# Performance work log

Measured on AMD Instinct MI355X. Metric: run time of the kernel, lower is better.

Reference implementation:

```python
import jax, jax.numpy as jnp
import numpy as np

B, S, DIM = 1, 2048, 4096
N_HEADS, N_KV_HEADS = 32, 8
HEAD_DIM = DIM // N_HEADS            # 128
N_REP = N_HEADS // N_KV_HEADS        # 4
Q_SIZE = N_HEADS * HEAD_DIM          # 4096
KV_SIZE = N_KV_HEADS * HEAD_DIM      # 1024


def setup_inputs() -> dict:
    key = jax.random.key(0)
    ks = jax.random.split(key, 5)
    x = jax.random.normal(ks[0], (B, S, DIM), dtype=jnp.float32)
    # RoPE tables: freqs_cis[s, j] = exp(i * s * theta_j), theta_j = 10000^(-2j/head_dim)
    theta = 10000.0 ** (-jnp.arange(0, HEAD_DIM, 2, dtype=jnp.float32) / HEAD_DIM)
    ang = jnp.arange(S, dtype=jnp.float32)[:, None] * theta[None, :]  # [S, HEAD_DIM//2]
    freqs_cos = jnp.cos(ang)
    freqs_sin = jnp.sin(ang)
    # causal additive mask [1,1,S,S]
    causal = jnp.tril(jnp.ones((S, S), dtype=bool))
    mask = jnp.where(causal, 0.0, -1e9).astype(jnp.float32)[None, None]
    wqkv = jax.random.normal(ks[1], (Q_SIZE + 2 * KV_SIZE, DIM), dtype=jnp.float32) * (DIM ** -0.5)
    wo = jax.random.normal(ks[2], (DIM, Q_SIZE), dtype=jnp.float32) * (Q_SIZE ** -0.5)
    return {"x": x, "freqs_cos": freqs_cos, "freqs_sin": freqs_sin, "mask": mask,
            "wqkv": wqkv, "wo": wo}


def _apply_rope(t, cos, sin):
    # t: [B, S, H, D]; cos/sin: [S, D//2]  (complex multiply on (even, odd) pairs)
    b, s, h, d = t.shape
    tp = t.reshape(b, s, h, d // 2, 2)
    t0, t1 = tp[..., 0], tp[..., 1]
    c = cos[None, :, None, :]
    sn = sin[None, :, None, :]
    out = jnp.stack([t0 * c - t1 * sn, t0 * sn + t1 * c], axis=-1)
    return out.reshape(b, s, h, d)


def reference(x, freqs_cos, freqs_sin, mask, wqkv, wo):
    bsz, seqlen, _ = x.shape
    qkv = jnp.einsum('bsd,od->bso', x, wqkv)  # fused QKV projection
    xq = qkv[..., :Q_SIZE].reshape(bsz, seqlen, N_HEADS, HEAD_DIM)
    xk = qkv[..., Q_SIZE:Q_SIZE + KV_SIZE].reshape(bsz, seqlen, N_KV_HEADS, HEAD_DIM)
    xv = qkv[..., Q_SIZE + KV_SIZE:].reshape(bsz, seqlen, N_KV_HEADS, HEAD_DIM)
    # rotary embedding on q, k
    xq = _apply_rope(xq, freqs_cos, freqs_sin)
    xk = _apply_rope(xk, freqs_cos, freqs_sin)
    # cache insertion (prefill: cache == current k/v), layout [B, KVH, S, D]
    cache_k = jnp.swapaxes(xk, 1, 2)
    cache_v = jnp.swapaxes(xv, 1, 2)
    # GQA repeat_kv -> [B, H, S, D]
    keys = jnp.repeat(cache_k, N_REP, axis=1)
    values = jnp.repeat(cache_v, N_REP, axis=1)
    # scores: einsum 'ijkl,ikml->ikjm' with xq [b,s,h,d], keys [b,h,t,d] -> [b,h,s,t]
    scores = jnp.einsum('bshd,bhtd->bhst', xq, keys) / jnp.sqrt(jnp.float32(HEAD_DIM))
    scores = scores + mask
    scores = jax.nn.softmax(scores.astype(jnp.float32), axis=-1).astype(xq.dtype)
    out = jnp.einsum('bhst,bhtd->bhsd', scores, values)  # [B, H, S, D]
    out = jnp.swapaxes(out, 1, 2).reshape(bsz, seqlen, Q_SIZE)
    return jnp.einsum('bso,do->bsd', out, wo)
```

## Files before the change

### kernel.cpp

```cpp
#include <hip/hip_runtime.h>
#include <hip/hip_bf16.h>
#include <cstdint>
#include <cstddef>


typedef __attribute__((ext_vector_type(4)))  float    f32x4;
typedef __attribute__((ext_vector_type(16))) float    f32x16;
typedef __attribute__((ext_vector_type(8)))  __bf16   bf16x8;
typedef __attribute__((ext_vector_type(4)))  __bf16   bf16x4;
typedef __attribute__((ext_vector_type(2)))  __bf16   bf16x2;
typedef __attribute__((ext_vector_type(4)))  uint32_t u32x4;

typedef const __attribute__((address_space(1))) void* gaddr_t;
typedef __attribute__((address_space(3))) void*       laddr_t;

#define S_LEN   2048
#define DIM_    4096
#define NHEADS  32
#define NKV     8
#define HD      128
#define QKV_LD  6144
#define KOFF    4096
#define VOFF    5120

#define EXP2F(x) __builtin_amdgcn_exp2f(x)

__global__ void cvt_f32_bf16(const float* __restrict__ in, __bf16* __restrict__ out, int n4) {
  int idx = blockIdx.x * blockDim.x + threadIdx.x;
  int stride = gridDim.x * blockDim.x;
  for (int i = idx; i < n4; i += stride) {
    float4 v = reinterpret_cast<const float4*>(in)[i];
    bf16x4 o;
    o[0] = (__bf16)v.x; o[1] = (__bf16)v.y; o[2] = (__bf16)v.z; o[3] = (__bf16)v.w;
    reinterpret_cast<bf16x4*>(out)[i] = o;
  }
}

__global__ void rope_kernel(__bf16* __restrict__ qkv, const float* __restrict__ fc,
                            const float* __restrict__ fs) {
  int tid = blockIdx.x * 256 + threadIdx.x;
  int i = tid & 63;
  int t = tid >> 6;
  int h = t % 40;
  int s = t / 40;
  int col = (h < NHEADS) ? (h * HD + 2 * i) : (KOFF + (h - NHEADS) * HD + 2 * i);
  size_t off = (size_t)s * QKV_LD + col;
  float c = fc[s * 64 + i], sn = fs[s * 64 + i];
  bf16x2 v = *reinterpret_cast<bf16x2*>(&qkv[off]);
  float t0 = (float)v[0], t1 = (float)v[1];
  bf16x2 o;
  o[0] = (__bf16)(t0 * c - t1 * sn);
  o[1] = (__bf16)(t0 * sn + t1 * c);
  *reinterpret_cast<bf16x2*>(&qkv[off]) = o;
}

__device__ __forceinline__ void stage64x(const __bf16* __restrict__ P, int ld, int row0,
                                         int kt, char* dst, int tid) {
#pragma unroll
  for (int j = 0; j < 2; ++j) {
    int c = j * 256 + tid;
    int r = c >> 3, g = c & 7;
    const __bf16* src = P + (size_t)(row0 + r) * ld + kt * 64 + ((g ^ (r & 7)) * 8);
    __builtin_amdgcn_global_load_lds((gaddr_t)src,
        (laddr_t)(dst + j * 4096 + (tid & ~63) * 16), 16, 0, 0);
  }
}

template <int KH, bool VM>
__device__ __forceinline__ void phase32(const __bf16* __restrict__ Ab,
                                        const __bf16* __restrict__ Bb,
                                        f32x16 (&acc)[2][2],
                                        int wm, int wn, int l31, int hi, int tid,
                                        const __bf16* __restrict__ SP, int sld,
                                        int srow0, char* sdst, int kt, bool st) {
  bf16x8 af[2][2], bfr[2][2];
#pragma unroll
  for (int mi = 0; mi < 2; ++mi) {
    int R = wm * 64 + mi * 32 + l31;
#pragma unroll
    for (int k2 = 0; k2 < 2; ++k2)
      af[mi][k2] = *reinterpret_cast<const bf16x8*>(
          (const char*)Ab + R * 128 + (((KH * 4 + k2 * 2 + hi) ^ (R & 7)) * 16));
  }
#pragma unroll
  for (int ni = 0; ni < 2; ++ni) {
    int R = wn * 64 + ni * 32 + l31;
#pragma unroll
    for (int k2 = 0; k2 < 2; ++k2)
      bfr[ni][k2] = *reinterpret_cast<const bf16x8*>(
          (const char*)Bb + R * 128 + (((KH * 4 + k2 * 2 + hi) ^ (R & 7)) * 16));
  }
  if (st) {
    stage64x(SP, sld, srow0, kt, sdst, tid);
    stage64x(SP, sld, srow0 + 64, kt, sdst + 8192, tid);
  }
  __builtin_amdgcn_s_barrier();
  asm volatile("s_waitcnt lgkmcnt(0)" ::: "memory");
  __builtin_amdgcn_sched_barrier(0);
  __builtin_amdgcn_s_setprio(1);
#pragma unroll
  for (int k2 = 0; k2 < 2; ++k2)
#pragma unroll
    for (int mi = 0; mi < 2; ++mi)
#pragma unroll
      for (int ni = 0; ni < 2; ++ni)
        acc[mi][ni] = __builtin_amdgcn_mfma_f32_32x32x16_bf16(af[mi][k2], bfr[ni][k2],
                                                              acc[mi][ni], 0, 0, 0);
  __builtin_amdgcn_s_setprio(0);
  if (VM) asm volatile("s_waitcnt vmcnt(0)" ::: "memory");
  __builtin_amdgcn_s_barrier();
}

template <int MB, int NPX, typename OutT>
__global__ __launch_bounds__(256, 2) void gemm32(const __bf16* __restrict__ A,
                                                 const __bf16* __restrict__ B,
                                                 OutT* __restrict__ C, int K,
                                                 int lda, int ldb, int ldc) {
  __shared__ __align__(16) __bf16 As[2][128 * 64];
  __shared__ __align__(16) __bf16 Bs[2][128 * 64];
  const int tid = threadIdx.x;
  const int lane = tid & 63, l31 = lane & 31, hi = lane >> 5, w = tid >> 6;
  const int wm = w >> 1, wn = w & 1;
  const int bid = blockIdx.x, xcd = bid & 7, lid = bid >> 3;
  const int m0 = (lid % MB) * 128;
  const int n0 = (xcd * NPX + lid / MB) * 128;

  f32x16 acc[2][2] = {};

  stage64x(A, lda, m0, 0, (char*)As[0], tid);
  stage64x(A, lda, m0 + 64, 0, (char*)As[0] + 8192, tid);
  stage64x(B, ldb, n0, 0, (char*)Bs[0], tid);
  stage64x(B, ldb, n0 + 64, 0, (char*)Bs[0] + 8192, tid);
  asm volatile("s_waitcnt vmcnt(0)" ::: "memory");
  __builtin_amdgcn_s_barrier();

  const int ntiles = K >> 6;
  for (int t = 0; t < ntiles; ++t) {
    const int cur = t & 1;
    const __bf16* Ab = As[cur];
    const __bf16* Bb = Bs[cur];
    char* dA = (char*)As[1 - cur];
    char* dB = (char*)Bs[1 - cur];
    const bool st = (t + 1 < ntiles);
    phase32<0, false>(Ab, Bb, acc, wm, wn, l31, hi, tid, A, lda, m0, dA, t + 1, st);
    phase32<1, true >(Ab, Bb, acc, wm, wn, l31, hi, tid, B, ldb, n0, dB, t + 1, st);
  }

#pragma unroll
  for (int mi = 0; mi < 2; ++mi)
#pragma unroll
    for (int ni = 0; ni < 2; ++ni)
#pragma unroll
      for (int e = 0; e < 16; ++e) {
        int row = m0 + wm * 64 + mi * 32 + (e & 3) + 8 * (e >> 2) + 4 * hi;
        int col = n0 + wn * 64 + ni * 32 + l31;
        C[(size_t)row * ldc + col] = (OutT)acc[mi][ni][e];
      }
}

__device__ inline uint32_t pack2(float a, float b) {
  bf16x2 t; t[0] = (__bf16)a; t[1] = (__bf16)b;
  return __builtin_bit_cast(uint32_t, t);
}

__global__ __launch_bounds__(256, 2) void attn_kernel(const __bf16* __restrict__ qkv,
                                                      __bf16* __restrict__ out) {
  __shared__ __align__(16) __bf16 Ks[2][64 * 128];
  __shared__ __align__(16) __bf16 Vt[2][128][72];
  const int tid = threadIdx.x;
  const int lane = tid & 63, l31 = lane & 31, hi = lane >> 5, wq = tid >> 6;
  const int head = blockIdx.x & 31;
  const int g = blockIdx.x >> 5;
  const int qt = (g < 8) ? (15 - g) : (g - 8);
  const int q0 = qt * 128;
  const int nt = 2 * qt + 2;
  const int kvh = head >> 2;
  const float sc2 = 0.08838834764831845f * 1.44269504089f;
  const int qr = q0 + wq * 32 + l31;

  bf16x8 vr[2][2];

  auto stage_k = [&](int tt, int buf) {
#pragma unroll
    for (int i = 0; i < 4; ++i) {
      int c = i * 256 + tid;
      int r = c >> 4, gg = c & 15;
      const __bf16* gk = qkv + (size_t)(tt * 64 + r) * QKV_LD + KOFF + kvh * HD + ((gg ^ (r & 7)) * 8);
      __builtin_amdgcn_global_load_lds((gaddr_t)gk,
          (laddr_t)((char*)Ks[buf] + (tid & ~63) * 16 + i * 4096), 16, 0, 0);
    }
  };
  auto load_v = [&](int tt) {
#pragma unroll
    for (int i = 0; i < 2; ++i) {
      int task = i * 256 + tid;
      int p = task >> 4, cg = task & 15;
      const __bf16* vp = qkv + (size_t)(tt * 64 + 2 * p) * QKV_LD + VOFF + kvh * HD + cg * 8;
      vr[i][0] = *reinterpret_cast<const bf16x8*>(vp);
      vr[i][1] = *reinterpret_cast<const bf16x8*>(vp + QKV_LD);
    }
  };
  auto write_v = [&](int buf) {
#pragma unroll
    for (int i = 0; i < 2; ++i) {
      int task = i * 256 + tid;
      int p = task >> 4, cg = task & 15;
#pragma unroll
      for (int e0 = 0; e0 < 8; ++e0) {
        int e = e0 ^ (lane & 7);
        bf16x2 pkv; pkv[0] = vr[i][0][e]; pkv[1] = vr[i][1][e];
        *reinterpret_cast<bf16x2*>(&Vt[buf][cg * 8 + e][2 * p]) = pkv;
      }
    }
  };

  bf16x8 qf[8];
  {
    const __bf16* qp = qkv + (size_t)qr * QKV_LD + head * HD + hi * 8;
#pragma unroll
    for (int ks = 0; ks < 8; ++ks) qf[ks] = *reinterpret_cast<const bf16x8*>(qp + ks * 16);
  }
  f32x16 o[4] = {};
  float m_run = -3e38f, l_run = 0.f;

  stage_k(0, 0); load_v(0); write_v(0);

  for (int t = 0; t < nt; ++t) {
    const int cur = t & 1;
    __syncthreads();
    if (t + 1 < nt) { stage_k(t + 1, 1 - cur); load_v(t + 1); }

    f32x16 st[2];
#pragma unroll
    for (int sub = 0; sub < 2; ++sub) {
      f32x16 acc = {};
      int r = sub * 32 + l31;
#pragma unroll
      for (int ks = 0; ks < 8; ++ks) {
        int gg = (ks * 2 + hi) ^ (r & 7);
        bf16x8 kf = *reinterpret_cast<const bf16x8*>((char*)Ks[cur] + r * 256 + gg * 16);
        acc = __builtin_amdgcn_mfma_f32_32x32x16_bf16(kf, qf[ks], acc, 0, 0, 0);
      }
      st[sub] = acc;
    }
#pragma unroll
    for (int sub = 0; sub < 2; ++sub)
#pragma unroll
      for (int e = 0; e < 16; ++e) st[sub][e] *= sc2;
    if (t >= nt - 2) {
      const int kv0 = t * 64;
#pragma unroll
      for (int sub = 0; sub < 2; ++sub)
#pragma unroll
        for (int e = 0; e < 16; ++e) {
          int kvg = kv0 + sub * 32 + (e & 3) + 8 * (e >> 2) + 4 * hi;
          if (kvg > qr) st[sub][e] = -1e30f;
        }
    }
    float pm = st[0][0];
#pragma unroll
    for (int e = 1; e < 16; ++e) pm = fmaxf(pm, st[0][e]);
#pragma unroll
    for (int e = 0; e < 16; ++e) pm = fmaxf(pm, st[1][e]);
    pm = fmaxf(pm, __shfl_xor(pm, 32));
    if (!__all(pm - m_run <= 8.f)) {
      float mn = fmaxf(m_run, pm);
      float fsc = EXP2F(m_run - mn);
      m_run = mn;
      l_run *= fsc;
#pragma unroll
      for (int dt = 0; dt < 4; ++dt)
#pragma unroll
        for (int e = 0; e < 16; ++e) o[dt][e] *= fsc;
    }
    float rs = 0.f;
#pragma unroll
    for (int sub = 0; sub < 2; ++sub)
#pragma unroll
      for (int e = 0; e < 16; ++e) {
        float p = EXP2F(st[sub][e] - m_run);
        st[sub][e] = p;
        rs += p;
      }
    rs += __shfl_xor(rs, 32);
    l_run += rs;

    uint32_t pk[16];
#pragma unroll
    for (int sub = 0; sub < 2; ++sub)
#pragma unroll
      for (int i = 0; i < 8; ++i)
        pk[sub * 8 + i] = pack2(st[sub][2 * i], st[sub][2 * i + 1]);
    uint32_t rv[8];
#pragma unroll
    for (int m = 0; m < 8; ++m) {
      int base = 4 * (m >> 1) + (m & 1);
      uint32_t snd = hi ? pk[base] : pk[base + 2];
      rv[m] = __shfl_xor(snd, 32);
    }
    bf16x8 pf[4];
#pragma unroll
    for (int tt = 0; tt < 4; ++tt) {
      u32x4 wv;
      wv[0] = hi ? rv[2 * tt]     : pk[4 * tt];
      wv[1] = hi ? rv[2 * tt + 1] : pk[4 * tt + 1];
      wv[2] = hi ? pk[4 * tt + 2] : rv[2 * tt];
      wv[3] = hi ? pk[4 * tt + 3] : rv[2 * tt + 1];
      pf[tt] = __builtin_bit_cast(bf16x8, wv);
    }
#pragma unroll
    for (int dt = 0; dt < 4; ++dt) {
      int dr = dt * 32 + l31;
#pragma unroll
      for (int tt = 0; tt < 4; ++tt) {
        bf16x8 vf = *reinterpret_cast<const bf16x8*>((char*)&Vt[cur][0][0] + dr * 144 + tt * 32 + hi * 16);
        o[dt] = __builtin_amdgcn_mfma_f32_32x32x16_bf16(vf, pf[tt], o[dt], 0, 0, 0);
      }
    }
    if (t + 1 < nt) write_v(1 - cur);
  }

  float inv = 1.f / l_run;
  __bf16* scr = &Ks[0][0] + wq * 1280;
  const int qq = lane >> 1, part = lane & 1;
#pragma unroll
  for (int dt = 0; dt < 4; ++dt) {
    __syncthreads();
#pragma unroll
    for (int i = 0; i < 8; ++i) {
      int d0 = (2 * i & 3) + 8 * (i >> 1) + 4 * hi;
      bf16x2 prr;
      prr[0] = (__bf16)(o[dt][2 * i] * inv);
      prr[1] = (__bf16)(o[dt][2 * i + 1] * inv);
      *reinterpret_cast<bf16x2*>(scr + l31 * 40 + d0) = prr;
    }
    __syncthreads();
    bf16x8 r0 = *reinterpret_cast<const bf16x8*>(scr + qq * 40 + part * 16);
    bf16x8 r1 = *reinterpret_cast<const bf16x8*>(scr + qq * 40 + part * 16 + 8);
    __bf16* op = out + (size_t)(q0 + wq * 32 + qq) * DIM_ + head * HD + dt * 32 + part * 16;
    *reinterpret_cast<bf16x8*>(op) = r0;
    *reinterpret_cast<bf16x8*>(op + 8) = r1;
  }
}

extern "C" void kernel_launch(void* const* d_in, const int* in_sizes, int n_in,
                              void* d_out, int out_size, void* d_ws, size_t ws_size,
                              hipStream_t stream) {
  (void)in_sizes; (void)n_in; (void)out_size; (void)ws_size;
  const float* x    = (const float*)d_in[0];
  const float* fc   = (const float*)d_in[1];
  const float* fs   = (const float*)d_in[2];
  const float* wqkv = (const float*)d_in[4];
  const float* wo   = (const float*)d_in[5];
  float* out = (float*)d_out;

  char* ws = (char*)d_ws;
  __bf16* xb    = (__bf16*)(ws);
  __bf16* wqkvb = (__bf16*)(ws + 16777216);
  __bf16* wob   = (__bf16*)(ws + 67108864);
  __bf16* qkv   = (__bf16*)(ws + 100663296);
  __bf16* attnO = xb;

  cvt_f32_bf16<<<2048, 256, 0, stream>>>(x,    xb,    (S_LEN * DIM_) / 4);
  cvt_f32_bf16<<<2048, 256, 0, stream>>>(wqkv, wqkvb, (6144 * DIM_) / 4);
  cvt_f32_bf16<<<2048, 256, 0, stream>>>(wo,   wob,   (DIM_ * DIM_) / 4);

  gemm32<16, 6, __bf16><<<768, 256, 0, stream>>>(xb, wqkvb, qkv, DIM_, DIM_, DIM_, QKV_LD);

  rope_kernel<<<(S_LEN * 40 * 64) / 256, 256, 0, stream>>>(qkv, fc, fs);

  attn_kernel<<<512, 256, 0, stream>>>(qkv, attnO);

  gemm32<16, 4, float><<<512, 256, 0, stream>>>(attnO, wob, out, DIM_, DIM_, DIM_, DIM_);
}
```

Baseline: 372.8 us.

## Enlarge GEMM tiles to 256-row blocks with 512-thread, 8-wave split-phase pipeline

Replaces the 128x128 GEMM with a 512-thread kernel that computes 256x256 (QKV) or 256x128 (output projection) tiles. Each wave now owns a larger accumulator block, which raises reuse of fragments loaded from LDS. Staging is split across two phases with partial vmcnt waits, so loads for the next K tile overlap compute. Grid sizes drop to 192 and 256 blocks, which risks leaving CUs underused on a 256-CU part and raises register and LDS pressure.

```diff
diff --git a/kernel.cpp b/kernel.cpp
--- a/kernel.cpp
+++ b/kernel.cpp
@@ -54,106 +54,160 @@
   *reinterpret_cast<bf16x2*>(&qkv[off]) = o;
 }
 
-__device__ __forceinline__ void stage64x(const __bf16* __restrict__ P, int ld, int row0,
-                                         int kt, char* dst, int tid) {
-#pragma unroll
-  for (int j = 0; j < 2; ++j) {
-    int c = j * 256 + tid;
-    int r = c >> 3, g = c & 7;
-    const __bf16* src = P + (size_t)(row0 + r) * ld + kt * 64 + ((g ^ (r & 7)) * 8);
-    __builtin_amdgcn_global_load_lds((gaddr_t)src,
-        (laddr_t)(dst + j * 4096 + (tid & ~63) * 16), 16, 0, 0);
-  }
-}
-
-template <int KH, bool VM>
-__device__ __forceinline__ void phase32(const __bf16* __restrict__ Ab,
-                                        const __bf16* __restrict__ Bb,
-                                        f32x16 (&acc)[2][2],
-                                        int wm, int wn, int l31, int hi, int tid,
-                                        const __bf16* __restrict__ SP, int sld,
-                                        int srow0, char* sdst, int kt, bool st) {
-  bf16x8 af[2][2], bfr[2][2];
+template <int N> __device__ __forceinline__ void vmwait() {
+  if constexpr (N == 0) asm volatile("s_waitcnt vmcnt(0)" ::: "memory");
+  else if constexpr (N == 2) asm volatile("s_waitcnt vmcnt(2)" ::: "memory");
+  else asm volatile("s_waitcnt vmcnt(4)" ::: "memory");
+}
+
+__device__ __forceinline__ void stg(const __bf16* __restrict__ P, int ld, int grow0,
+                                    int kt, char* dst, int tid) {
+  int r = tid >> 3, g = tid & 7;
+  int row = grow0 + r;
+  const __bf16* src = P + (size_t)row * ld + kt * 64 + ((g ^ (row & 7)) * 8);
+  __builtin_amdgcn_global_load_lds((gaddr_t)src,
+      (laddr_t)(dst + (tid & ~63) * 16), 16, 0, 0);
+}
+
+template <int NI, int WAIT, bool ST>
+__device__ __forceinline__ void phase0(const __bf16* __restrict__ Ab,
+                                       const __bf16* __restrict__ Bb,
+                                       f32x16 (&acc)[4][NI], bf16x8 (&bfr)[NI][4],
+                                       int wm, int wn, int l31, int hi, int tid,
+                                       const __bf16* __restrict__ A, int lda, int m0, char* dA,
+                                       const __bf16* __restrict__ B, int ldb, int n0, char* dB,
+                                       int kt) {
+  vmwait<WAIT>();
+  __builtin_amdgcn_s_barrier();
+  bf16x8 af[2][4];
 #pragma unroll
   for (int mi = 0; mi < 2; ++mi) {
-    int R = wm * 64 + mi * 32 + l31;
-#pragma unroll
-    for (int k2 = 0; k2 < 2; ++k2)
-      af[mi][k2] = *reinterpret_cast<const bf16x8*>(
-          (const char*)Ab + R * 128 + (((KH * 4 + k2 * 2 + hi) ^ (R & 7)) * 16));
-  }
-#pragma unroll
-  for (int ni = 0; ni < 2; ++ni) {
-    int R = wn * 64 + ni * 32 + l31;
-#pragma unroll
-    for (int k2 = 0; k2 < 2; ++k2)
-      bfr[ni][k2] = *reinterpret_cast<const bf16x8*>(
-          (const char*)Bb + R * 128 + (((KH * 4 + k2 * 2 + hi) ^ (R & 7)) * 16));
-  }
-  if (st) {
-    stage64x(SP, sld, srow0, kt, sdst, tid);
-    stage64x(SP, sld, srow0 + 64, kt, sdst + 8192, tid);
-  }
-  __builtin_amdgcn_s_barrier();
+    int R = wm * 128 + mi * 32 + l31;
+#pragma unroll
+    for (int s = 0; s < 4; ++s)
+      af[mi][s] = *reinterpret_cast<const bf16x8*>(
+          (const char*)Ab + R * 128 + (((s * 2 + hi) ^ (R & 7)) * 16));
+  }
+#pragma unroll
+  for (int ni = 0; ni < NI; ++ni) {
+    int R = wn * (NI * 32) + ni * 32 + l31;
+#pragma unroll
+    for (int s = 0; s < 4; ++s)
+      bfr[ni][s] = *reinterpret_cast<const bf16x8*>(
+          (const char*)Bb + R * 128 + (((s * 2 + hi) ^ (R & 7)) * 16));
+  }
+  if constexpr (ST) {
+    stg(A, lda, m0,       kt, dA,             tid);
+    stg(A, lda, m0 + 128, kt, dA + 128 * 128, tid);
+    stg(B, ldb, n0,       kt, dB,             tid);
+    stg(B, ldb, n0 + 64,  kt, dB + 64 * 128,  tid);
+  }
   asm volatile("s_waitcnt lgkmcnt(0)" ::: "memory");
   __builtin_amdgcn_sched_barrier(0);
   __builtin_amdgcn_s_setprio(1);
 #pragma unroll
-  for (int k2 = 0; k2 < 2; ++k2)
+  for (int s = 0; s < 4; ++s)
 #pragma unroll
     for (int mi = 0; mi < 2; ++mi)
 #pragma unroll
-      for (int ni = 0; ni < 2; ++ni)
-        acc[mi][ni] = __builtin_amdgcn_mfma_f32_32x32x16_bf16(af[mi][k2], bfr[ni][k2],
+      for (int ni = 0; ni < NI; ++ni)
+        acc[mi][ni] = __builtin_amdgcn_mfma_f32_32x32x16_bf16(af[mi][s], bfr[ni][s],
                                                               acc[mi][ni], 0, 0, 0);
   __builtin_amdgcn_s_setprio(0);
-  if (VM) asm volatile("s_waitcnt vmcnt(0)" ::: "memory");
+}
+
+template <int NI, int WAIT, bool ST>
+__device__ __forceinline__ void phase1(const __bf16* __restrict__ Ab,
+                                       f32x16 (&acc)[4][NI], bf16x8 (&bfr)[NI][4],
+                                       int wm, int l31, int hi, int tid,
+                                       const __bf16* __restrict__ A, int lda, int m0, char* dA,
+                                       const __bf16* __restrict__ B, int ldb, int n0, char* dB,
+                                       int kt) {
+  vmwait<WAIT>();
   __builtin_amdgcn_s_barrier();
-}
-
-template <int MB, int NPX, typename OutT>
-__global__ __launch_bounds__(256, 2) void gemm32(const __bf16* __restrict__ A,
-                                                 const __bf16* __restrict__ B,
-                                                 OutT* __restrict__ C, int K,
-                                                 int lda, int ldb, int ldc) {
-  __shared__ __align__(16) __bf16 As[2][128 * 64];
-  __shared__ __align__(16) __bf16 Bs[2][128 * 64];
+  bf16x8 af[2][4];
+#pragma unroll
+  for (int mi = 0; mi < 2; ++mi) {
+    int R = wm * 128 + 64 + mi * 32 + l31;
+#pragma unroll
+    for (int s = 0; s < 4; ++s)
+      af[mi][s] = *reinterpret_cast<const bf16x8*>(
+          (const char*)Ab + R * 128 + (((s * 2 + hi) ^ (R & 7)) * 16));
+  }
+  if constexpr (ST) {
+    if constexpr (NI == 2) {
+      stg(B, ldb, n0 + 128, kt, dB + 128 * 128, tid);
+      stg(B, ldb, n0 + 192, kt, dB + 192 * 128, tid);
+    }
+    stg(A, lda, m0 + 64,  kt, dA + 64 * 128,  tid);
+    stg(A, lda, m0 + 192, kt, dA + 192 * 128, tid);
+  }
+  asm volatile("s_waitcnt lgkmcnt(0)" ::: "memory");
+  __builtin_amdgcn_sched_barrier(0);
+  __builtin_amdgcn_s_setprio(1);
+#pragma unroll
+  for (int s = 0; s < 4; ++s)
+#pragma unroll
+    for (int mi = 0; mi < 2; ++mi)
+#pragma unroll
+      for (int ni = 0; ni < NI; ++ni)
+        acc[2 + mi][ni] = __builtin_amdgcn_mfma_f32_32x32x16_bf16(af[mi][s], bfr[ni][s],
+                                                                  acc[2 + mi][ni], 0, 0, 0);
+  __builtin_amdgcn_s_setprio(0);
+}
+
+template <int NI, int MB, int NPX, typename OutT>
+__global__ __launch_bounds__(512, 2) void gemmQ(const __bf16* __restrict__ A,
+                                                const __bf16* __restrict__ B,
+                                                OutT* __restrict__ C, int K,
+                                                int lda, int ldb, int ldc) {
+  __shared__ __align__(16) __bf16 As[2][256 * 64];
+  __shared__ __align__(16) __bf16 Bs[2][NI * 128 * 64];
   const int tid = threadIdx.x;
   const int lane = tid & 63, l31 = lane & 31, hi = lane >> 5, w = tid >> 6;
-  const int wm = w >> 1, wn = w & 1;
+  const int wm = w >> 2, wn = w & 3;
   const int bid = blockIdx.x, xcd = bid & 7, lid = bid >> 3;
-  const int m0 = (lid % MB) * 128;
-  const int n0 = (xcd * NPX + lid / MB) * 128;
-
-  f32x16 acc[2][2] = {};
-
-  stage64x(A, lda, m0, 0, (char*)As[0], tid);
-  stage64x(A, lda, m0 + 64, 0, (char*)As[0] + 8192, tid);
-  stage64x(B, ldb, n0, 0, (char*)Bs[0], tid);
-  stage64x(B, ldb, n0 + 64, 0, (char*)Bs[0] + 8192, tid);
-  asm volatile("s_waitcnt vmcnt(0)" ::: "memory");
-  __builtin_amdgcn_s_barrier();
-
-  const int ntiles = K >> 6;
-  for (int t = 0; t < ntiles; ++t) {
+  const int m0 = (lid % MB) * 256;
+  const int n0 = (xcd * NPX + lid / MB) * (NI * 128);
+
+  f32x16 acc[4][NI] = {};
+  bf16x8 bfr[NI][4];
+
+  stg(A, lda, m0,       0, (char*)As[0],             tid);
+  stg(A, lda, m0 + 128, 0, (char*)As[0] + 128 * 128, tid);
+  stg(B, ldb, n0,       0, (char*)Bs[0],             tid);
+  stg(B, ldb, n0 + 64,  0, (char*)Bs[0] + 64 * 128,  tid);
+  if constexpr (NI == 2) {
+    stg(B, ldb, n0 + 128, 0, (char*)Bs[0] + 128 * 128, tid);
+    stg(B, ldb, n0 + 192, 0, (char*)Bs[0] + 192 * 128, tid);
+  }
+  stg(A, lda, m0 + 64,  0, (char*)As[0] + 64 * 128,  tid);
+  stg(A, lda, m0 + 192, 0, (char*)As[0] + 192 * 128, tid);
+
+  const int nt = K >> 6;
+  for (int t = 0; t < nt; ++t) {
     const int cur = t & 1;
     const __bf16* Ab = As[cur];
     const __bf16* Bb = Bs[cur];
     char* dA = (char*)As[1 - cur];
     char* dB = (char*)Bs[1 - cur];
-    const bool st = (t + 1 < ntiles);
-    phase32<0, false>(Ab, Bb, acc, wm, wn, l31, hi, tid, A, lda, m0, dA, t + 1, st);
-    phase32<1, true >(Ab, Bb, acc, wm, wn, l31, hi, tid, B, ldb, n0, dB, t + 1, st);
-  }
-
-#pragma unroll
-  for (int mi = 0; mi < 2; ++mi)
-#pragma unroll
-    for (int ni = 0; ni < 2; ++ni)
+    if (t + 1 < nt) {
+      phase0<NI, 2, true>(Ab, Bb, acc, bfr, wm, wn, l31, hi, tid, A, lda, m0, dA, B, ldb, n0, dB, t + 1);
+      phase1<NI, 4, true>(Ab, acc, bfr, wm, l31, hi, tid, A, lda, m0, dA, B, ldb, n0, dB, t + 1);
+    } else {
+      phase0<NI, 2, false>(Ab, Bb, acc, bfr, wm, wn, l31, hi, tid, A, lda, m0, dA, B, ldb, n0, dB, 0);
+      phase1<NI, 0, false>(Ab, acc, bfr, wm, l31, hi, tid, A, lda, m0, dA, B, ldb, n0, dB, 0);
+    }
+  }
+
+#pragma unroll
+  for (int mi = 0; mi < 4; ++mi)
+#pragma unroll
+    for (int ni = 0; ni < NI; ++ni)
 #pragma unroll
       for (int e = 0; e < 16; ++e) {
-        int row = m0 + wm * 64 + mi * 32 + (e & 3) + 8 * (e >> 2) + 4 * hi;
-        int col = n0 + wn * 64 + ni * 32 + l31;
+        int row = m0 + wm * 128 + mi * 32 + (e & 3) + 8 * (e >> 2) + 4 * hi;
+        int col = n0 + wn * (NI * 32) + ni * 32 + l31;
         C[(size_t)row * ldc + col] = (OutT)acc[mi][ni][e];
       }
 }
@@ -365,11 +419,11 @@
   cvt_f32_bf16<<<2048, 256, 0, stream>>>(wqkv, wqkvb, (6144 * DIM_) / 4);
   cvt_f32_bf16<<<2048, 256, 0, stream>>>(wo,   wob,   (DIM_ * DIM_) / 4);
 
-  gemm32<16, 6, __bf16><<<768, 256, 0, stream>>>(xb, wqkvb, qkv, DIM_, DIM_, DIM_, QKV_LD);
+  gemmQ<2, 8, 3, __bf16><<<192, 512, 0, stream>>>(xb, wqkvb, qkv, DIM_, DIM_, DIM_, QKV_LD);
 
   rope_kernel<<<(S_LEN * 40 * 64) / 256, 256, 0, stream>>>(qkv, fc, fs);
 
   attn_kernel<<<512, 256, 0, stream>>>(qkv, attnO);
 
-  gemm32<16, 4, float><<<512, 256, 0, stream>>>(attnO, wob, out, DIM_, DIM_, DIM_, DIM_);
-}
+  gemmQ<1, 8, 4, float><<<256, 512, 0, stream>>>(attnO, wob, out, DIM_, DIM_, DIM_, DIM_);
+}
```

New measurement: 1.322 ms. 255% more time.

## Replace GEMMs with 512-thread 256-wide tile kernel using 8-phase pipelined staging

Applied to the files above, without the earlier changes.

Swaps the 128x128, 256-thread GEMM for a templated 512-thread kernel with larger tiles (256x256 for QKV, 128x256 for the output projection). It uses 16x16x32 MFMAs and splits each k-tile into quadrant phases, with half-tile staging and partial vmcnt waits so global-to-LDS loads overlap compute more finely. The goal is more data reuse per block and fewer full memory stalls. In exchange, far fewer blocks are launched (192 and 256 on a 256-CU part), which risks under-filling the GPU or leaving a tail, and the larger tiles raise register and LDS pressure.

```diff
diff --git a/kernel.cpp b/kernel.cpp
--- a/kernel.cpp
+++ b/kernel.cpp
@@ -54,108 +54,145 @@
   *reinterpret_cast<bf16x2*>(&qkv[off]) = o;
 }
 
-__device__ __forceinline__ void stage64x(const __bf16* __restrict__ P, int ld, int row0,
+template <int N> __device__ __forceinline__ void vmw() {
+  if constexpr (N == 3)      asm volatile("s_waitcnt vmcnt(3)" ::: "memory");
+  else if constexpr (N == 4) asm volatile("s_waitcnt vmcnt(4)" ::: "memory");
+  else if constexpr (N == 6) asm volatile("s_waitcnt vmcnt(6)" ::: "memory");
+  else if constexpr (N == 8) asm volatile("s_waitcnt vmcnt(8)" ::: "memory");
+  else if constexpr (N == 0) asm volatile("s_waitcnt vmcnt(0)" ::: "memory");
+}
+
+__device__ __forceinline__ void stg64(const __bf16* __restrict__ P, int ld, int grow0,
+                                      int kt, char* dst, int tid) {
+  int r = tid >> 3, g = tid & 7;
+  int row = grow0 + r;
+  const __bf16* src = P + (size_t)row * ld + kt * 64 + ((g ^ (row & 7)) * 8);
+  __builtin_amdgcn_global_load_lds((gaddr_t)src,
+      (laddr_t)(dst + (tid & ~63) * 16), 16, 0, 0);
+}
+
+template <int NR64>
+__device__ __forceinline__ void stg_half(const __bf16* __restrict__ P, int ld, int grow0,
                                          int kt, char* dst, int tid) {
 #pragma unroll
-  for (int j = 0; j < 2; ++j) {
-    int c = j * 256 + tid;
-    int r = c >> 3, g = c & 7;
-    const __bf16* src = P + (size_t)(row0 + r) * ld + kt * 64 + ((g ^ (r & 7)) * 8);
-    __builtin_amdgcn_global_load_lds((gaddr_t)src,
-        (laddr_t)(dst + j * 4096 + (tid & ~63) * 16), 16, 0, 0);
-  }
-}
-
-template <int KH, bool VM>
-__device__ __forceinline__ void phase32(const __bf16* __restrict__ Ab,
-                                        const __bf16* __restrict__ Bb,
-                                        f32x16 (&acc)[2][2],
-                                        int wm, int wn, int l31, int hi, int tid,
-                                        const __bf16* __restrict__ SP, int sld,
-                                        int srow0, char* sdst, int kt, bool st) {
-  bf16x8 af[2][2], bfr[2][2];
-#pragma unroll
-  for (int mi = 0; mi < 2; ++mi) {
-    int R = wm * 64 + mi * 32 + l31;
-#pragma unroll
-    for (int k2 = 0; k2 < 2; ++k2)
-      af[mi][k2] = *reinterpret_cast<const bf16x8*>(
-          (const char*)Ab + R * 128 + (((KH * 4 + k2 * 2 + hi) ^ (R & 7)) * 16));
-  }
-#pragma unroll
-  for (int ni = 0; ni < 2; ++ni) {
-    int R = wn * 64 + ni * 32 + l31;
-#pragma unroll
-    for (int k2 = 0; k2 < 2; ++k2)
-      bfr[ni][k2] = *reinterpret_cast<const bf16x8*>(
-          (const char*)Bb + R * 128 + (((KH * 4 + k2 * 2 + hi) ^ (R & 7)) * 16));
-  }
-  if (st) {
-    stage64x(SP, sld, srow0, kt, sdst, tid);
-    stage64x(SP, sld, srow0 + 64, kt, sdst + 8192, tid);
-  }
+  for (int h = 0; h < NR64; ++h) stg64(P, ld, grow0 + h * 64, kt, dst + h * 8192, tid);
+}
+
+template <int BM, int BN, int QM, int QN, int VW, int SNR>
+__device__ __forceinline__ void do_phase(const __bf16* __restrict__ Ab,
+                                         const __bf16* __restrict__ Bb,
+                                         f32x4 (&acc)[2 * (BM / 64)][2 * (BN / 128)],
+                                         int wm, int wn, int l15, int hi, int tid,
+                                         const __bf16* __restrict__ SP, int sld,
+                                         int sgrow0, int skt, char* sdst, bool doSt) {
+  constexpr int FM2 = BM / 64;
+  constexpr int FN2 = BN / 128;
+  bf16x8 af[FM2][2], bf[FN2][2];
+#pragma unroll
+  for (int fm = 0; fm < FM2; ++fm) {
+    int R = QM * (BM / 2) + wm * (BM / 4) + fm * 16 + l15;
+#pragma unroll
+    for (int kk = 0; kk < 2; ++kk)
+      af[fm][kk] = *reinterpret_cast<const bf16x8*>(
+          (const char*)Ab + R * 128 + (((kk * 4 + hi) ^ (R & 7)) * 16));
+  }
+#pragma unroll
+  for (int fn = 0; fn < FN2; ++fn) {
+    int R = QN * (BN / 2) + wn * (BN / 8) + fn * 16 + l15;
+#pragma unroll
+    for (int kk = 0; kk < 2; ++kk)
+      bf[fn][kk] = *reinterpret_cast<const bf16x8*>(
+          (const char*)Bb + R * 128 + (((kk * 4 + hi) ^ (R & 7)) * 16));
+  }
+  if (doSt) stg_half<SNR>(SP, sld, sgrow0, skt, sdst, tid);
   __builtin_amdgcn_s_barrier();
   asm volatile("s_waitcnt lgkmcnt(0)" ::: "memory");
   __builtin_amdgcn_sched_barrier(0);
   __builtin_amdgcn_s_setprio(1);
 #pragma unroll
-  for (int k2 = 0; k2 < 2; ++k2)
-#pragma unroll
-    for (int mi = 0; mi < 2; ++mi)
-#pragma unroll
-      for (int ni = 0; ni < 2; ++ni)
-        acc[mi][ni] = __builtin_amdgcn_mfma_f32_32x32x16_bf16(af[mi][k2], bfr[ni][k2],
-                                                              acc[mi][ni], 0, 0, 0);
+  for (int kk = 0; kk < 2; ++kk)
+#pragma unroll
+    for (int fm = 0; fm < FM2; ++fm)
+#pragma unroll
+      for (int fn = 0; fn < FN2; ++fn)
+        acc[QM * FM2 + fm][QN * FN2 + fn] = __builtin_amdgcn_mfma_f32_16x16x32_bf16(
+            af[fm][kk], bf[fn][kk], acc[QM * FM2 + fm][QN * FN2 + fn], 0, 0, 0);
   __builtin_amdgcn_s_setprio(0);
-  if (VM) asm volatile("s_waitcnt vmcnt(0)" ::: "memory");
+  if constexpr (VW >= 0) vmw<VW>();
   __builtin_amdgcn_s_barrier();
 }
 
-template <int MB, int NPX, typename OutT>
-__global__ __launch_bounds__(256, 2) void gemm32(const __bf16* __restrict__ A,
-                                                 const __bf16* __restrict__ B,
-                                                 OutT* __restrict__ C, int K,
-                                                 int lda, int ldb, int ldc) {
-  __shared__ __align__(16) __bf16 As[2][128 * 64];
-  __shared__ __align__(16) __bf16 Bs[2][128 * 64];
+template <int BM, int BN, int MB, int NX, typename OutT>
+__global__ __launch_bounds__(512) void gemm8p(const __bf16* __restrict__ A,
+                                              const __bf16* __restrict__ B,
+                                              OutT* __restrict__ C, int K,
+                                              int lda, int ldb, int ldc) {
+  constexpr int AH = BM / 128;
+  constexpr int BH = BN / 128;
+  constexpr int W0 = AH + BH;
+  constexpr int W1 = 2 * AH + 2 * BH;
+  constexpr int W2 = 2 * AH + BH;
+  constexpr int FM2 = BM / 64, FN2 = BN / 128;
+  __shared__ __align__(16) __bf16 As[2][BM * 64];
+  __shared__ __align__(16) __bf16 Bs[2][BN * 64];
   const int tid = threadIdx.x;
-  const int lane = tid & 63, l31 = lane & 31, hi = lane >> 5, w = tid >> 6;
-  const int wm = w >> 1, wn = w & 1;
+  const int l15 = tid & 15, hi = (tid >> 4) & 3, w = tid >> 6;
+  const int wm = w >> 2, wn = w & 3;
   const int bid = blockIdx.x, xcd = bid & 7, lid = bid >> 3;
-  const int m0 = (lid % MB) * 128;
-  const int n0 = (xcd * NPX + lid / MB) * 128;
-
-  f32x16 acc[2][2] = {};
-
-  stage64x(A, lda, m0, 0, (char*)As[0], tid);
-  stage64x(A, lda, m0 + 64, 0, (char*)As[0] + 8192, tid);
-  stage64x(B, ldb, n0, 0, (char*)Bs[0], tid);
-  stage64x(B, ldb, n0 + 64, 0, (char*)Bs[0] + 8192, tid);
-  asm volatile("s_waitcnt vmcnt(0)" ::: "memory");
+  const int m0 = (lid % MB) * BM;
+  const int n0 = (xcd * NX + lid / MB) * BN;
+
+  f32x4 acc[2 * FM2][2 * FN2] = {};
+
+  char* A0 = (char*)As[0]; char* A1 = (char*)As[1];
+  char* B0 = (char*)Bs[0]; char* B1 = (char*)Bs[1];
+  const int Ah = (BM / 2) * 128;
+  const int Bh = (BN / 2) * 128;
+
+  stg_half<AH>(A, lda, m0,          0, A0,      tid);
+  stg_half<BH>(B, ldb, n0,          0, B0,      tid);
+  stg_half<AH>(A, lda, m0 + BM / 2, 0, A0 + Ah, tid);
+  stg_half<BH>(B, ldb, n0 + BN / 2, 0, B0 + Bh, tid);
+  stg_half<AH>(A, lda, m0,          1, A1,      tid);
+  stg_half<BH>(B, ldb, n0,          1, B1,      tid);
+  vmw<W0>();
   __builtin_amdgcn_s_barrier();
 
-  const int ntiles = K >> 6;
-  for (int t = 0; t < ntiles; ++t) {
-    const int cur = t & 1;
-    const __bf16* Ab = As[cur];
-    const __bf16* Bb = Bs[cur];
-    char* dA = (char*)As[1 - cur];
-    char* dB = (char*)Bs[1 - cur];
-    const bool st = (t + 1 < ntiles);
-    phase32<0, false>(Ab, Bb, acc, wm, wn, l31, hi, tid, A, lda, m0, dA, t + 1, st);
-    phase32<1, true >(Ab, Bb, acc, wm, wn, l31, hi, tid, B, ldb, n0, dB, t + 1, st);
-  }
-
-#pragma unroll
-  for (int mi = 0; mi < 2; ++mi)
-#pragma unroll
-    for (int ni = 0; ni < 2; ++ni)
-#pragma unroll
-      for (int e = 0; e < 16; ++e) {
-        int row = m0 + wm * 64 + mi * 32 + (e & 3) + 8 * (e >> 2) + 4 * hi;
-        int col = n0 + wn * 64 + ni * 32 + l31;
-        C[(size_t)row * ldc + col] = (OutT)acc[mi][ni][e];
-      }
+  const int nt = K >> 6;
+  for (int it = 0; it < nt; it += 2) {
+    const bool s2 = (it + 2 < nt), s3 = (it + 3 < nt);
+    do_phase<BM, BN, 0, 0, W2, AH>(As[0], Bs[0], acc, wm, wn, l15, hi, tid,
+                                   A, lda, m0 + BM / 2, it + 1, A1 + Ah, true);
+    do_phase<BM, BN, 0, 1, -1, BH>(As[0], Bs[0], acc, wm, wn, l15, hi, tid,
+                                   B, ldb, n0 + BN / 2, it + 1, B1 + Bh, true);
+    do_phase<BM, BN, 1, 0, -1, AH>(As[0], Bs[0], acc, wm, wn, l15, hi, tid,
+                                   A, lda, m0, it + 2, A0, s2);
+    do_phase<BM, BN, 1, 1, W1, BH>(As[0], Bs[0], acc, wm, wn, l15, hi, tid,
+                                   B, ldb, n0, it + 2, B0, s2);
+    do_phase<BM, BN, 0, 0, W2, AH>(As[1], Bs[1], acc, wm, wn, l15, hi, tid,
+                                   A, lda, m0 + BM / 2, it + 2, A0 + Ah, s2);
+    do_phase<BM, BN, 0, 1, -1, BH>(As[1], Bs[1], acc, wm, wn, l15, hi, tid,
+                                   B, ldb, n0 + BN / 2, it + 2, B0 + Bh, s2);
+    do_phase<BM, BN, 1, 0, -1, AH>(As[1], Bs[1], acc, wm, wn, l15, hi, tid,
+                                   A, lda, m0, it + 3, A1, s3);
+    do_phase<BM, BN, 1, 1, W1, BH>(As[1], Bs[1], acc, wm, wn, l15, hi, tid,
+                                   B, ldb, n0, it + 3, B1, s3);
+  }
+
+#pragma unroll
+  for (int qm = 0; qm < 2; ++qm)
+#pragma unroll
+    for (int fm = 0; fm < FM2; ++fm)
+#pragma unroll
+      for (int qn = 0; qn < 2; ++qn)
+#pragma unroll
+        for (int fn = 0; fn < FN2; ++fn)
+#pragma unroll
+          for (int j = 0; j < 4; ++j) {
+            int row = m0 + qm * (BM / 2) + wm * (BM / 4) + fm * 16 + hi * 4 + j;
+            int col = n0 + qn * (BN / 2) + wn * (BN / 8) + fn * 16 + l15;
+            C[(size_t)row * ldc + col] = (OutT)acc[qm * FM2 + fm][qn * FN2 + fn][j];
+          }
 }
 
 __device__ inline uint32_t pack2(float a, float b) {
@@ -365,11 +402,11 @@
   cvt_f32_bf16<<<2048, 256, 0, stream>>>(wqkv, wqkvb, (6144 * DIM_) / 4);
   cvt_f32_bf16<<<2048, 256, 0, stream>>>(wo,   wob,   (DIM_ * DIM_) / 4);
 
-  gemm32<16, 6, __bf16><<<768, 256, 0, stream>>>(xb, wqkvb, qkv, DIM_, DIM_, DIM_, QKV_LD);
+  gemm8p<256, 256, 8, 3, __bf16><<<192, 512, 0, stream>>>(xb, wqkvb, qkv, DIM_, DIM_, DIM_, QKV_LD);
 
   rope_kernel<<<(S_LEN * 40 * 64) / 256, 256, 0, stream>>>(qkv, fc, fs);
 
   attn_kernel<<<512, 256, 0, stream>>>(qkv, attnO);
 
-  gemm32<16, 4, float><<<512, 256, 0, stream>>>(attnO, wob, out, DIM_, DIM_, DIM_, DIM_);
-}
+  gemm8p<128, 256, 16, 2, float><<<256, 512, 0, stream>>>(attnO, wob, out, DIM_, DIM_, DIM_, DIM_);
+}
```

Result: slower. 388.3 us (+4.2%).
